# Optimization experiments

Hardware: AMD Instinct MI355X
Metric: run time of the kernel (lower is better)

## Reference

```python
import jax, jax.numpy as jnp
import numpy as np
from jax import lax

E, H = 512, 1024
V_SRC, V_DST = 32000, 32000
T_SRC, T_TGT, B = 64, 64, 64
PAD = 0


def setup_inputs() -> dict:
    key = jax.random.key(0)
    ks = jax.random.split(key, 32)
    def p(i, shape, s=0.02):
        return (jax.random.normal(ks[i], shape) * s).astype(jnp.float32)
    lens = jnp.sort(jax.random.randint(ks[0], (B,), T_SRC // 2, T_SRC + 1))[::-1]
    return {
        "source_padded": jax.random.randint(ks[1], (T_SRC, B), 0, V_SRC).astype(jnp.int32),
        "target_padded": jax.random.randint(ks[2], (T_TGT, B), 0, V_DST).astype(jnp.int32),
        "source_lengths": lens.at[0].set(T_SRC).astype(jnp.int32),
        "src_embed": p(3, (V_SRC, E)),
        "dst_embed": p(4, (V_DST, E)),
        "W_ih_f": p(5, (4 * H, E)), "W_hh_f": p(6, (4 * H, H)),
        "b_ih_f": p(7, (4 * H,)), "b_hh_f": p(8, (4 * H,)),
        "W_ih_b": p(9, (4 * H, E)), "W_hh_b": p(10, (4 * H, H)),
        "b_ih_b": p(11, (4 * H,)), "b_hh_b": p(12, (4 * H,)),
        "W_ih_d": p(13, (4 * H, E + H)), "W_hh_d": p(14, (4 * H, H)),
        "b_ih_d": p(15, (4 * H,)), "b_hh_d": p(16, (4 * H,)),
        "W_hproj": p(17, (H, 2 * H)), "W_cproj": p(18, (H, 2 * H)),
        "W_att": p(19, (H, 2 * H)), "W_comb": p(20, (H, 3 * H)),
        "W_vocab": p(21, (V_DST, H)),
    }


def _lstm_cell(x, h, c, Wih, Whh, bih, bhh):
    # PyTorch gate order: i, f, g, o
    g = x @ Wih.T + bih + h @ Whh.T + bhh
    i, f, gg, o = jnp.split(g, 4, axis=-1)
    c2 = jax.nn.sigmoid(f) * c + jax.nn.sigmoid(i) * jnp.tanh(gg)
    h2 = jax.nn.sigmoid(o) * jnp.tanh(c2)
    return h2, c2


def _nmt_forward(source_padded, target_padded, source_lengths,
                 src_embed, dst_embed,
                 W_ih_f, W_hh_f, b_ih_f, b_hh_f,
                 W_ih_b, W_hh_b, b_ih_b, b_hh_b,
                 W_ih_d, W_hh_d, b_ih_d, b_hh_d,
                 W_hproj, W_cproj, W_att, W_comb, W_vocab):
    T, Bsz = source_padded.shape
    dt = src_embed.dtype
    x = src_embed[source_padded]                      # [T, B, E]
    mask = jnp.arange(T)[:, None] < source_lengths[None, :]  # [T, B] valid

    def make_step(Wih, Whh, bih, bhh):
        def step(carry, inp):
            h, c = carry
            xt, mt = inp
            h2, c2 = _lstm_cell(xt, h, c, Wih, Whh, bih, bhh)
            m = mt[:, None]
            hn = jnp.where(m, h2, h)   # hold state past sequence end (packed semantics)
            cn = jnp.where(m, c2, c)
            return (hn, cn), jnp.where(m, h2, jnp.zeros_like(h2))  # pad outputs are zero
        return step

    z = jnp.zeros((Bsz, H), dt)
    (hf, cf), out_f = lax.scan(make_step(W_ih_f, W_hh_f, b_ih_f, b_hh_f), (z, z), (x, mask))
    (hb, cb), out_b_rev = lax.scan(make_step(W_ih_b, W_hh_b, b_ih_b, b_hh_b), (z, z), (x[::-1], mask[::-1]))
    out_b = out_b_rev[::-1]

    enc_hiddens = jnp.concatenate([out_f, out_b], axis=-1).transpose(1, 0, 2)  # [B, T, 2H]
    h0 = jnp.concatenate([hf, hb], axis=-1) @ W_hproj.T  # [B, H]
    c0 = jnp.concatenate([cf, cb], axis=-1) @ W_cproj.T
    enc_proj = enc_hiddens @ W_att.T                     # [B, T, H]
    pad_mask = ~mask.T                                   # [B, T] True at <pad>

    y = dst_embed[target_padded[:-1]]                    # [Tt-1, B, E]

    def dec_step(carry, yt):
        h, c, o_prev = carry
        ybar = jnp.concatenate([yt, o_prev], axis=-1)    # [B, E+H]
        h2, c2 = _lstm_cell(ybar, h, c, W_ih_d, W_hh_d, b_ih_d, b_hh_d)
        e = jnp.einsum('bth,bh->bt', enc_proj, h2)       # attention scores
        e = jnp.where(pad_mask, -jnp.inf, e)
        alpha = jax.nn.softmax(e, axis=1)
        a = jnp.einsum('bt,btd->bd', alpha, enc_hiddens)  # context [B, 2H]
        O = jnp.tanh(jnp.concatenate([a, h2], axis=-1) @ W_comb.T)  # dropout = identity (eval)
        return (h2, c2, O), O

    _, outs = lax.scan(dec_step, (h0, c0, z), y)         # [Tt-1, B, H]

    P = jax.nn.log_softmax(outs @ W_vocab.T, axis=-1)    # [Tt-1, B, V]
    gold = jnp.take_along_axis(P, target_padded[1:][..., None], axis=-1)[..., 0]
    tmask = (target_padded[1:] != PAD).astype(P.dtype)
    return (gold * tmask).sum(axis=0)                    # [B]


def reference(source_padded, target_padded, source_lengths,
              src_embed, dst_embed,
              W_ih_f, W_hh_f, b_ih_f, b_hh_f,
              W_ih_b, W_hh_b, b_ih_b, b_hh_b,
              W_ih_d, W_hh_d, b_ih_d, b_hh_d,
              W_hproj, W_cproj, W_att, W_comb, W_vocab):
    return _nmt_forward(source_padded, target_padded, source_lengths,
                        src_embed, dst_embed,
                        W_ih_f, W_hh_f, b_ih_f, b_hh_f,
                        W_ih_b, W_hh_b, b_ih_b, b_hh_b,
                        W_ih_d, W_hh_d, b_ih_d, b_hh_d,
                        W_hproj, W_cproj, W_att, W_comb, W_vocab)
```

## Files before the change

### kernel.cpp

```cpp
#include <hip/hip_runtime.h>

typedef __attribute__((ext_vector_type(8))) short short8;
typedef __attribute__((ext_vector_type(4))) float f32x4;
typedef __attribute__((ext_vector_type(4))) unsigned int uint4v;
typedef unsigned short u16;

#define DEVI static __device__ __forceinline__

constexpr int TTm = 64;
constexpr int BBm = 64;
constexpr int EEm = 512;
constexpr int HHm = 1024;
constexpr int GGm = 4096;
constexpr int TDm = 63;

DEVI u16 f2b(float f) {
  unsigned u = __builtin_bit_cast(unsigned, f);
  return (u16)((u + 0x7fffu + ((u >> 16) & 1u)) >> 16);
}
DEVI float b2f(u16 h) { return __builtin_bit_cast(float, (unsigned)h << 16); }
DEVI float sigm(float x) { return 1.0f / (1.0f + __expf(-x)); }
DEVI float tanh_(float x) { return 1.0f - 2.0f / (1.0f + __expf(2.0f * x)); }

DEVI short8 cvt8(const float* p) {
  f32x4 x0 = *(const f32x4*)p;
  f32x4 x1 = *(const f32x4*)(p + 4);
  short8 r;
#pragma unroll
  for (int i = 0; i < 4; ++i) { r[i] = (short)f2b(x0[i]); r[i + 4] = (short)f2b(x1[i]); }
  return r;
}
DEVI void stage32_f32(short* dst, const float* src) {
#pragma unroll
  for (int i = 0; i < 4; ++i) *(short8*)&dst[i * 8] = cvt8(src + i * 8);
}
DEVI void stage32_b16(short* dst, const u16* src) {
#pragma unroll
  for (int i = 0; i < 4; ++i) *(uint4v*)&dst[i * 8] = *(const uint4v*)(src + i * 8);
}

DEVI void gbar(unsigned* flags, unsigned phase) {
  __syncthreads();
  if (threadIdx.x == 0) {
    __builtin_amdgcn_fence(__ATOMIC_RELEASE, "agent");
    __hip_atomic_store(&flags[blockIdx.x * 16], phase, __ATOMIC_RELAXED,
                       __HIP_MEMORY_SCOPE_AGENT);
  }
  if (threadIdx.x < 64) {
    const int i0 = threadIdx.x * 4;
    for (;;) {
      int ok = 1;
#pragma unroll
      for (int i = 0; i < 4; ++i) {
        unsigned v = __hip_atomic_load(&flags[(i0 + i) * 16], __ATOMIC_RELAXED,
                                       __HIP_MEMORY_SCOPE_AGENT);
        ok &= (v >= phase);
      }
      if (__all(ok)) break;
      __builtin_amdgcn_s_sleep(1);
    }
    __builtin_amdgcn_fence(__ATOMIC_ACQUIRE, "agent");
  }
  __syncthreads();
}

DEVI void mfma_bk64(const short* As, const short* Bs, f32x4 acc[4][2], int wv, int ln) {
  const int l15 = ln & 15;
#pragma unroll
  for (int ks = 0; ks < 64; ks += 32) {
    const int kq = ks + ((ln >> 4) << 3);
    short8 b0 = *(const short8*)&Bs[(wv * 32 + l15) * 72 + kq];
    short8 b1 = *(const short8*)&Bs[(wv * 32 + 16 + l15) * 72 + kq];
#pragma unroll
    for (int mt = 0; mt < 4; ++mt) {
      short8 a = *(const short8*)&As[(mt * 16 + l15) * 72 + kq];
      acc[mt][0] = __builtin_amdgcn_mfma_f32_16x16x32_bf16(a, b0, acc[mt][0], 0, 0, 0);
      acc[mt][1] = __builtin_amdgcn_mfma_f32_16x16x32_bf16(a, b1, acc[mt][1], 0, 0, 0);
    }
  }
}

__global__ void k_zero(uint4v* p, int n16) {
  int i = blockIdx.x * blockDim.x + threadIdx.x;
  uint4v z = {0u, 0u, 0u, 0u};
  for (; i < n16; i += gridDim.x * blockDim.x) p[i] = z;
}

__global__ void k_cvt_all(const float* Wihf, const float* Wihb, const float* Whhf,
                          const float* Whhb, const float* Wihd, const float* Whhd,
                          const float* Watt, const float* Whp, const float* Wcp,
                          const float* Wcomb, const float* Wvoc,
                          u16* o_ihf, u16* o_ihb, u16* o_hhf, u16* o_hhb,
                          u16* o_cat1, u16* o_cat2,
                          u16* o_att, u16* o_hp, u16* o_cp, u16* o_comb, u16* o_voc) {
  long i = (long)blockIdx.x * blockDim.x + threadIdx.x;
  const long stride = (long)gridDim.x * blockDim.x;
  for (; i < 65273856L; i += stride) {
    long r = i;
    if (r < 2097152) { o_ihf[r] = f2b(Wihf[r]); continue; } r -= 2097152;
    if (r < 2097152) { o_ihb[r] = f2b(Wihb[r]); continue; } r -= 2097152;
    if (r < 4194304) { o_hhf[r] = f2b(Whhf[r]); continue; } r -= 4194304;
    if (r < 4194304) { o_hhb[r] = f2b(Whhb[r]); continue; } r -= 4194304;
    if (r < 2097152) {
      long g = r >> 9, c = r & 511;
      o_cat1[r] = f2b(Wihd[g * 1536 + c]); continue;
    } r -= 2097152;
    if (r < 8388608) {
      long g = r >> 11, c = r & 2047;
      o_cat2[r] = f2b(c < 1024 ? Wihd[g * 1536 + 512 + c] : Whhd[g * 1024 + (c - 1024)]);
      continue;
    } r -= 8388608;
    if (r < 2097152) { o_att[r] = f2b(Watt[r]); continue; } r -= 2097152;
    if (r < 2097152) { o_hp[r] = f2b(Whp[r]); continue; } r -= 2097152;
    if (r < 2097152) { o_cp[r] = f2b(Wcp[r]); continue; } r -= 2097152;
    if (r < 3145728) { o_comb[r] = f2b(Wcomb[r]); continue; } r -= 3145728;
    o_voc[r] = f2b(Wvoc[r]);
  }
}

__global__ __launch_bounds__(128) void k_pre(
    const int* tok, const float* emb, const u16* W,
    const float* bi, const float* bh, u16* pre) {
  __shared__ short As[64 * 72], Bs[64 * 72];
  const int rt = blockIdx.x, ct = blockIdx.y;
  const int tid = threadIdx.x, wv = tid >> 6, sr = tid & 63, seg = tid >> 6;
  const int token = tok[rt * 64 + sr];
  const float* arow = emb + (long)token * EEm;
  const u16* brow = W + (long)(ct * 64 + sr) * EEm;
  f32x4 acc[4][2] = {};
  for (int k0 = 0; k0 < EEm; k0 += 64) {
    __syncthreads();
    stage32_f32(&As[sr * 72 + seg * 32], arow + k0 + seg * 32);
    stage32_b16(&Bs[sr * 72 + seg * 32], brow + k0 + seg * 32);
    __syncthreads();
    mfma_bk64(As, Bs, acc, wv, sr);
  }
  const int l15 = sr & 15, q = sr >> 4;
#pragma unroll
  for (int nt = 0; nt < 2; ++nt) {
    const int col = ct * 64 + wv * 32 + nt * 16 + l15;
    const float bias = bi[col] + bh[col];
#pragma unroll
    for (int mt = 0; mt < 4; ++mt)
#pragma unroll
      for (int r = 0; r < 4; ++r)
        pre[(long)(rt * 64 + mt * 16 + q * 4 + r) * GGm + col] = f2b(acc[mt][nt][r] + bias);
  }
}

template <bool OUTB16>
__global__ __launch_bounds__(128) void k_gemm_plain(const u16* A, const u16* Bm,
                                                    void* C, int K, int ldb) {
  __shared__ short As[64 * 72], Bs[64 * 72];
  const int rt = blockIdx.x, ct = blockIdx.y;
  const int tid = threadIdx.x, wv = tid >> 6, sr = tid & 63, seg = tid >> 6;
  const u16* arow = A + (long)(rt * 64 + sr) * K;
  const u16* brow = Bm + (long)(ct * 64 + sr) * ldb;
  f32x4 acc[4][2] = {};
  for (int k0 = 0; k0 < K; k0 += 64) {
    __syncthreads();
    stage32_b16(&As[sr * 72 + seg * 32], arow + k0 + seg * 32);
    stage32_b16(&Bs[sr * 72 + seg * 32], brow + k0 + seg * 32);
    __syncthreads();
    mfma_bk64(As, Bs, acc, wv, sr);
  }
  const int l15 = sr & 15, q = sr >> 4, ldc = gridDim.y * 64;
#pragma unroll
  for (int nt = 0; nt < 2; ++nt) {
    const int col = ct * 64 + wv * 32 + nt * 16 + l15;
#pragma unroll
    for (int mt = 0; mt < 4; ++mt)
#pragma unroll
      for (int r = 0; r < 4; ++r) {
        const long idx = (long)(rt * 64 + mt * 16 + q * 4 + r) * ldc + col;
        if (OUTB16) ((u16*)C)[idx] = f2b(acc[mt][nt][r]);
        else        ((float*)C)[idx] = acc[mt][nt][r];
      }
  }
}

__global__ __launch_bounds__(256) void k_enc_all(
    const u16* __restrict__ Whhf, const u16* __restrict__ Whhb,
    const u16* __restrict__ pre_f, const u16* __restrict__ pre_b,
    const int* __restrict__ lens,
    u16* h_f, u16* h_b, u16* ench, u16* hcat, u16* ccat, unsigned* bar) {
  __shared__ float gshE[4 * 64 * 33];
  const int blk = blockIdx.x;
  const int dir = blk >> 7, jt = blk & 127, j0 = jt * 8;
  const u16* Whh = dir ? Whhb : Whhf;
  const u16* pre = dir ? pre_b : pre_f;
  u16* hbase = dir ? h_b : h_f;
  const int tid = threadIdx.x, wv = tid >> 6, ln = tid & 63;
  const int l15 = ln & 15, half = ln >> 4;
  short8 bf[8][2];
#pragma unroll
  for (int i = 0; i < 8; ++i) {
    const int k = (i * 4 + wv) * 32 + half * 8;
#pragma unroll
    for (int nt = 0; nt < 2; ++nt) {
      const int n = nt * 16 + l15, g = n >> 3, jj = n & 7;
      bf[i][nt] = *(const short8*)(Whh + (long)(g * 1024 + j0 + jj) * 1024 + k);
    }
  }
  const int cb = tid & 63, cj = tid >> 6;
  const int len_b = lens[cb];
  float creg[2] = {0.f, 0.f};
  for (int s = 0; s < 64; ++s) {
    const int t = dir ? (63 - s) : s;
    const u16* hcur = hbase + (s & 1) * 65536;
    u16* hnxt = hbase + ((s & 1) ^ 1) * 65536;
    f32x4 acc[4][2] = {};
#pragma unroll
    for (int i = 0; i < 8; ++i) {
      const int k = (i * 4 + wv) * 32 + half * 8;
#pragma unroll
      for (int mt = 0; mt < 4; ++mt) {
        short8 a = *(const short8*)(hcur + (mt * 16 + l15) * 1024 + k);
        acc[mt][0] = __builtin_amdgcn_mfma_f32_16x16x32_bf16(a, bf[i][0], acc[mt][0], 0, 0, 0);
        acc[mt][1] = __builtin_amdgcn_mfma_f32_16x16x32_bf16(a, bf[i][1], acc[mt][1], 0, 0, 0);
      }
    }
    __syncthreads();
#pragma unroll
    for (int mt = 0; mt < 4; ++mt)
#pragma unroll
      for (int nt = 0; nt < 2; ++nt)
#pragma unroll
        for (int r = 0; r < 4; ++r)
          gshE[wv * 2112 + (mt * 16 + half * 4 + r) * 33 + nt * 16 + l15] = acc[mt][nt][r];
    __syncthreads();
#pragma unroll
    for (int u = 0; u < 2; ++u) {
      const int jj = cj + u * 4, j = j0 + jj;
      float g4[4];
#pragma unroll
      for (int g = 0; g < 4; ++g) {
        const int n = g * 8 + jj;
        float v = gshE[cb * 33 + n] + gshE[2112 + cb * 33 + n] +
                  gshE[2 * 2112 + cb * 33 + n] + gshE[3 * 2112 + cb * 33 + n];
        v += b2f(pre[((long)t * 64 + cb) * GGm + g * 1024 + j]);
        g4[g] = v;
      }
      const float cold = creg[u];
      const float c2 = sigm(g4[1]) * cold + sigm(g4[0]) * tanh_(g4[2]);
      const float h2 = sigm(g4[3]) * tanh_(c2);
      const bool m = t < len_b;
      creg[u] = m ? c2 : cold;
      hnxt[cb * 1024 + j] = m ? f2b(h2) : hcur[cb * 1024 + j];
      ench[((long)cb * 64 + t) * 2048 + dir * 1024 + j] = f2b(m ? h2 : 0.f);
    }
    if (s < 63) gbar(bar, s + 1);
  }
#pragma unroll
  for (int u = 0; u < 2; ++u) {
    const int j = j0 + cj + u * 4;
    hcat[cb * 2048 + dir * 1024 + j] = hbase[cb * 1024 + j];
    ccat[cb * 2048 + dir * 1024 + j] = f2b(creg[u]);
  }
}

__global__ __launch_bounds__(256) void k_dec_all(
    const u16* __restrict__ Wcat2, const u16* __restrict__ Wcomb,
    const u16* __restrict__ y_pre, const u16* __restrict__ eproj,
    const u16* __restrict__ encW, const int* __restrict__ lens,
    u16* h_d, float* c_d, u16* o_b, u16* outs, unsigned* bar) {
  __shared__ float gsh[4 * 64 * 17];
  __shared__ float h2s[1024];
  __shared__ float part[256];
  __shared__ float alph[64];
  const int blk = blockIdx.x, tid = threadIdx.x, wv = tid >> 6, ln = tid & 63;
  const int l15 = ln & 15, half = ln >> 4;
  const int j0 = blk * 4;
  short8 bg[16];
#pragma unroll
  for (int i = 0; i < 16; ++i) {
    const int k = (i * 4 + wv) * 32 + half * 8;
    const int g = l15 >> 2, jj = l15 & 3;
    bg[i] = *(const short8*)(Wcat2 + (long)(g * 1024 + j0 + jj) * 2048 + k);
  }
  const int cb = tid & 63, cj = tid >> 6;
  const int ab = blk & 63, aq = blk >> 6;
  const int len_ab = lens[ab];
  float creg = c_d[cb * 1024 + j0 + cj];
  unsigned phase = 0;
  for (int t = 0; t < TDm; ++t) {
    const u16* hprev = h_d + (t & 1) * 65536;
    u16* hnew = h_d + ((t & 1) ^ 1) * 65536;
    f32x4 acc[4] = {};
#pragma unroll
    for (int i = 0; i < 16; ++i) {
      const int k = (i * 4 + wv) * 32 + half * 8;
      const u16* asrc = (k < 1024) ? (o_b + k) : (hprev + (k - 1024));
#pragma unroll
      for (int mt = 0; mt < 4; ++mt) {
        short8 a = *(const short8*)(asrc + (mt * 16 + l15) * 1024);
        acc[mt] = __builtin_amdgcn_mfma_f32_16x16x32_bf16(a, bg[i], acc[mt], 0, 0, 0);
      }
    }
    __syncthreads();
#pragma unroll
    for (int mt = 0; mt < 4; ++mt)
#pragma unroll
      for (int r = 0; r < 4; ++r)
        gsh[wv * 1088 + (mt * 16 + half * 4 + r) * 17 + l15] = acc[mt][r];
    __syncthreads();
    {
      float g4[4];
#pragma unroll
      for (int g = 0; g < 4; ++g) {
        const int n = g * 4 + cj;
        float v = gsh[cb * 17 + n] + gsh[1088 + cb * 17 + n] +
                  gsh[2 * 1088 + cb * 17 + n] + gsh[3 * 1088 + cb * 17 + n];
        v += b2f(y_pre[((long)t * 64 + cb) * GGm + g * 1024 + j0 + cj]);
        g4[g] = v;
      }
      const float c2 = sigm(g4[1]) * creg + sigm(g4[0]) * tanh_(g4[2]);
      const float h2 = sigm(g4[3]) * tanh_(c2);
      creg = c2;
      hnew[cb * 1024 + j0 + cj] = f2b(h2);
    }
    gbar(bar, ++phase);
    for (int i = tid; i < 1024; i += 256) h2s[i] = b2f(hnew[ab * 1024 + i]);
    __syncthreads();
    {
      const int tt = tid >> 2, qq = tid & 3;
      const u16* row = eproj + ((long)ab * 64 + tt) * 1024 + qq * 256;
      float a0 = 0.f;
      for (int i = 0; i < 256; i += 8) {
        uint4v v = *(const uint4v*)(row + i);
        const u16* pv = (const u16*)&v;
#pragma unroll
        for (int j = 0; j < 8; ++j) a0 += b2f(pv[j]) * h2s[qq * 256 + i + j];
      }
      part[tid] = a0;
    }
    __syncthreads();
    if (tid < 64) {
      float e = part[tid * 4] + part[tid * 4 + 1] + part[tid * 4 + 2] + part[tid * 4 + 3];
      e = (tid < len_ab) ? e : -INFINITY;
      float mx = e;
#pragma unroll
      for (int m = 1; m < 64; m <<= 1) mx = fmaxf(mx, __shfl_xor(mx, m));
      float p = __expf(e - mx);
      float s = p;
#pragma unroll
      for (int m = 1; m < 64; m <<= 1) s += __shfl_xor(s, m);
      alph[tid] = p / s;
    }
    __syncthreads();
    {
      const int j = aq * 256 + tid;
      float oa = 0.f;
      for (int tt = 0; tt < 64; ++tt) {
        const float al = alph[tt];
        if (al != 0.f) oa += al * b2f(encW[((long)ab * 64 + tt) * 1024 + j]);
      }
      float oh = 0.f;
      const u16* wrow = Wcomb + (long)j * 3072 + 2048;
      for (int k = 0; k < 1024; k += 8) {
        uint4v v = *(const uint4v*)(wrow + k);
        const u16* pv = (const u16*)&v;
#pragma unroll
        for (int jj = 0; jj < 8; ++jj) oh += b2f(pv[jj]) * h2s[k + jj];
      }
      const u16 ob = f2b(tanh_(oa + oh));
      o_b[ab * 1024 + j] = ob;
      outs[((long)t * 64 + ab) * 1024 + j] = ob;
    }
    if (t < TDm - 1) gbar(bar, ++phase);
  }
}

__global__ __launch_bounds__(128) void k_vocab(const u16* outs, const u16* Wvoc,
                                               float* sumexp) {
  __shared__ short As[64 * 72], Bs[64 * 72];
  const int vt = blockIdx.x, t = blockIdx.y;
  const int tid = threadIdx.x, wv = tid >> 6, sr = tid & 63, seg = tid >> 6;
  const u16* arow = outs + ((long)t * 64 + sr) * 1024;
  const u16* brow = Wvoc + (long)(vt * 64 + sr) * 1024;
  f32x4 acc[4][2] = {};
  for (int k0 = 0; k0 < 1024; k0 += 64) {
    __syncthreads();
    stage32_b16(&As[sr * 72 + seg * 32], arow + k0 + seg * 32);
    stage32_b16(&Bs[sr * 72 + seg * 32], brow + k0 + seg * 32);
    __syncthreads();
    mfma_bk64(As, Bs, acc, wv, sr);
  }
  const int l15 = sr & 15, q = sr >> 4;
#pragma unroll
  for (int mt = 0; mt < 4; ++mt)
#pragma unroll
    for (int r = 0; r < 4; ++r) {
      float e = __expf(acc[mt][0][r]) + __expf(acc[mt][1][r]);
      e += __shfl_xor(e, 1); e += __shfl_xor(e, 2);
      e += __shfl_xor(e, 4); e += __shfl_xor(e, 8);
      if (l15 == 0) atomicAdd(&sumexp[t * 64 + mt * 16 + q * 4 + r], e);
    }
}

__global__ __launch_bounds__(256) void k_gold(const u16* outs, const u16* Wvoc,
                                              const int* tgt, float* gold) {
  const int t = blockIdx.x;
  const int wv = threadIdx.x >> 6, ln = threadIdx.x & 63;
  for (int b = wv; b < 64; b += 4) {
    const int g = tgt[(t + 1) * 64 + b];
    const u16* o = outs + ((long)t * 64 + b) * 1024 + ln * 16;
    const u16* w = Wvoc + (long)g * 1024 + ln * 16;
    uint4v v0 = *(const uint4v*)o, v1 = *(const uint4v*)(o + 8);
    uint4v w0 = *(const uint4v*)w, w1 = *(const uint4v*)(w + 8);
    const u16 *pv0 = (const u16*)&v0, *pv1 = (const u16*)&v1;
    const u16 *pw0 = (const u16*)&w0, *pw1 = (const u16*)&w1;
    float acc = 0.f;
#pragma unroll
    for (int j = 0; j < 8; ++j)
      acc += b2f(pv0[j]) * b2f(pw0[j]) + b2f(pv1[j]) * b2f(pw1[j]);
#pragma unroll
    for (int m = 1; m < 64; m <<= 1) acc += __shfl_xor(acc, m);
    if (ln == 0) gold[t * 64 + b] = acc;
  }
}

__global__ void k_final(const float* gold, const float* sumexp, const int* tgt,
                        float* out) {
  const int b = threadIdx.x;
  float s = 0.f;
  for (int t = 0; t < TDm; ++t)
    if (tgt[(t + 1) * 64 + b] != 0)
      s += gold[t * 64 + b] - logf(sumexp[t * 64 + b]);
  out[b] = s;
}

extern "C" void kernel_launch(void* const* d_in, const int* in_sizes, int n_in,
                              void* d_out, int out_size, void* d_ws, size_t ws_size,
                              hipStream_t stream) {
  const int* src_tok = (const int*)d_in[0];
  const int* tgt_tok = (const int*)d_in[1];
  const int* lens    = (const int*)d_in[2];
  const float* semb  = (const float*)d_in[3];
  const float* demb  = (const float*)d_in[4];
  const float* Wihf  = (const float*)d_in[5];
  const float* Whhf  = (const float*)d_in[6];
  const float* bihf  = (const float*)d_in[7];
  const float* bhhf  = (const float*)d_in[8];
  const float* Wihb  = (const float*)d_in[9];
  const float* Whhb  = (const float*)d_in[10];
  const float* bihb  = (const float*)d_in[11];
  const float* bhhb  = (const float*)d_in[12];
  const float* Wihd  = (const float*)d_in[13];
  const float* Whhd  = (const float*)d_in[14];
  const float* bihd  = (const float*)d_in[15];
  const float* bhhd  = (const float*)d_in[16];
  const float* Whp   = (const float*)d_in[17];
  const float* Wcp   = (const float*)d_in[18];
  const float* Watt  = (const float*)d_in[19];
  const float* Wcomb = (const float*)d_in[20];
  const float* Wvoc  = (const float*)d_in[21];

  char* w = (char*)d_ws;
  auto alloc = [&](size_t bytes) { char* p = w; w += (bytes + 255) & ~(size_t)255; return p; };
  u16* h_f    = (u16*)alloc(262144);
  u16* h_b    = (u16*)alloc(262144);
  u16* o_b    = (u16*)alloc(131072);
  float* sume = (float*)alloc(16384);
  unsigned* barE = (unsigned*)alloc(16384);
  unsigned* barD = (unsigned*)alloc(16384);
  const int zero16 = (int)((w - (char*)h_f) / 16);
  float* gold   = (float*)alloc(16384);
  float* c_d    = (float*)alloc(262144);
  u16* h_d      = (u16*)alloc(262144);
  u16* hcat     = (u16*)alloc(262144);
  u16* ccat     = (u16*)alloc(262144);
  u16* Wb_ihf   = (u16*)alloc(4194304);
  u16* Wb_ihb   = (u16*)alloc(4194304);
  u16* Wb_hhf   = (u16*)alloc(8388608);
  u16* Wb_hhb   = (u16*)alloc(8388608);
  u16* Wb_cat1  = (u16*)alloc(4194304);
  u16* Wb_cat2  = (u16*)alloc(16777216);
  u16* Wb_att   = (u16*)alloc(4194304);
  u16* Wb_hp    = (u16*)alloc(4194304);
  u16* Wb_cp    = (u16*)alloc(4194304);
  u16* Wb_comb  = (u16*)alloc(6291456);
  u16* Wb_voc   = (u16*)alloc(65536000);
  u16* pre_f    = (u16*)alloc(33554432);
  u16* pre_b    = (u16*)alloc(33554432);
  u16* y_pre    = (u16*)alloc(33030144);
  u16* ench     = (u16*)alloc(16777216);
  u16* eproj    = (u16*)alloc(8388608);
  u16* encW     = (u16*)alloc(8388608);
  u16* outs     = (u16*)alloc(8257536);

  k_zero<<<dim3(128), dim3(256), 0, stream>>>((uint4v*)h_f, zero16);
  k_cvt_all<<<dim3(2048), dim3(256), 0, stream>>>(
      Wihf, Wihb, Whhf, Whhb, Wihd, Whhd, Watt, Whp, Wcp, Wcomb, Wvoc,
      Wb_ihf, Wb_ihb, Wb_hhf, Wb_hhb, Wb_cat1, Wb_cat2,
      Wb_att, Wb_hp, Wb_cp, Wb_comb, Wb_voc);
  k_pre<<<dim3(64, 64), dim3(128), 0, stream>>>(src_tok, semb, Wb_ihf, bihf, bhhf, pre_f);
  k_pre<<<dim3(64, 64), dim3(128), 0, stream>>>(src_tok, semb, Wb_ihb, bihb, bhhb, pre_b);
  k_pre<<<dim3(63, 64), dim3(128), 0, stream>>>(tgt_tok, demb, Wb_cat1, bihd, bhhd, y_pre);
  {
    void* args[] = {(void*)&Wb_hhf, (void*)&Wb_hhb, (void*)&pre_f, (void*)&pre_b,
                    (void*)&lens, (void*)&h_f, (void*)&h_b, (void*)&ench,
                    (void*)&hcat, (void*)&ccat, (void*)&barE};
    hipLaunchCooperativeKernel((void*)k_enc_all, dim3(256), dim3(256), args, 0, stream);
  }
  k_gemm_plain<true><<<dim3(1, 16), dim3(128), 0, stream>>>(hcat, Wb_hp, (void*)h_d, 2048, 2048);
  k_gemm_plain<false><<<dim3(1, 16), dim3(128), 0, stream>>>(ccat, Wb_cp, (void*)c_d, 2048, 2048);
  k_gemm_plain<true><<<dim3(64, 16), dim3(128), 0, stream>>>(ench, Wb_att, (void*)eproj, 2048, 2048);
  k_gemm_plain<true><<<dim3(64, 16), dim3(128), 0, stream>>>(ench, Wb_comb, (void*)encW, 2048, 3072);
  {
    void* args[] = {(void*)&Wb_cat2, (void*)&Wb_comb, (void*)&y_pre, (void*)&eproj,
                    (void*)&encW, (void*)&lens, (void*)&h_d, (void*)&c_d,
                    (void*)&o_b, (void*)&outs, (void*)&barD};
    hipLaunchCooperativeKernel((void*)k_dec_all, dim3(256), dim3(256), args, 0, stream);
  }
  k_vocab<<<dim3(500, 63), dim3(128), 0, stream>>>(outs, Wb_voc, sume);
  k_gold<<<dim3(63), dim3(256), 0, stream>>>(outs, Wb_voc, tgt_tok, gold);
  k_final<<<dim3(1), dim3(64), 0, stream>>>(gold, sume, tgt_tok, (float*)d_out);
}
```

Before: 9.233 ms.

## Replace fence-based grid barrier with write-through stores and per-step history buffers

Recurrent state buffers (encoder h, decoder h and o) change from ping-pong double buffers to full per-timestep history arrays, so each step writes to fresh addresses that no other block has cached. Cross-block stores go out as write-through system-scope global_store_short (sc0 sc1), which lets the grid barrier drop its agent-scope release and acquire fences in favour of a vmcnt wait. The intent is to cut the cache writeback and invalidate cost of the 64+126 grid barriers in the recurrent loops. In exchange it uses more workspace and relies on the fresh-address argument for correctness, since readers no longer do an acquire invalidate. The outs buffer now aliases the decoder o-history.

```diff
diff --git a/kernel.cpp b/kernel.cpp
--- a/kernel.cpp
+++ b/kernel.cpp
@@ -39,10 +39,15 @@
   for (int i = 0; i < 4; ++i) *(uint4v*)&dst[i * 8] = *(const uint4v*)(src + i * 8);
 }
 
+DEVI void st_sys_b16(u16* p, u16 v) {
+  unsigned d = v;
+  asm volatile("global_store_short %0, %1, off sc0 sc1" :: "v"(p), "v"(d) : "memory");
+}
+
 DEVI void gbar(unsigned* flags, unsigned phase) {
+  asm volatile("s_waitcnt vmcnt(0)" ::: "memory");
   __syncthreads();
   if (threadIdx.x == 0) {
-    __builtin_amdgcn_fence(__ATOMIC_RELEASE, "agent");
     __hip_atomic_store(&flags[blockIdx.x * 16], phase, __ATOMIC_RELAXED,
                        __HIP_MEMORY_SCOPE_AGENT);
   }
@@ -59,8 +64,8 @@
       if (__all(ok)) break;
       __builtin_amdgcn_s_sleep(1);
     }
-    __builtin_amdgcn_fence(__ATOMIC_ACQUIRE, "agent");
-  }
+  }
+  asm volatile("" ::: "memory");
   __syncthreads();
 }
 
@@ -183,13 +188,13 @@
     const u16* __restrict__ Whhf, const u16* __restrict__ Whhb,
     const u16* __restrict__ pre_f, const u16* __restrict__ pre_b,
     const int* __restrict__ lens,
-    u16* h_f, u16* h_b, u16* ench, u16* hcat, u16* ccat, unsigned* bar) {
+    u16* hist_f, u16* hist_b, u16* ench, u16* hcat, u16* ccat, unsigned* bar) {
   __shared__ float gshE[4 * 64 * 33];
   const int blk = blockIdx.x;
   const int dir = blk >> 7, jt = blk & 127, j0 = jt * 8;
   const u16* Whh = dir ? Whhb : Whhf;
   const u16* pre = dir ? pre_b : pre_f;
-  u16* hbase = dir ? h_b : h_f;
+  u16* hist = dir ? hist_b : hist_f;
   const int tid = threadIdx.x, wv = tid >> 6, ln = tid & 63;
   const int l15 = ln & 15, half = ln >> 4;
   short8 bf[8][2];
@@ -205,10 +210,11 @@
   const int cb = tid & 63, cj = tid >> 6;
   const int len_b = lens[cb];
   float creg[2] = {0.f, 0.f};
+  u16 hlast[2] = {0, 0};
   for (int s = 0; s < 64; ++s) {
     const int t = dir ? (63 - s) : s;
-    const u16* hcur = hbase + (s & 1) * 65536;
-    u16* hnxt = hbase + ((s & 1) ^ 1) * 65536;
+    const u16* hcur = hist + s * 65536;
+    u16* hnxt = hist + (s + 1) * 65536;
     f32x4 acc[4][2] = {};
 #pragma unroll
     for (int i = 0; i < 8; ++i) {
@@ -246,7 +252,9 @@
       const float h2 = sigm(g4[3]) * tanh_(c2);
       const bool m = t < len_b;
       creg[u] = m ? c2 : cold;
-      hnxt[cb * 1024 + j] = m ? f2b(h2) : hcur[cb * 1024 + j];
+      const u16 hv = m ? f2b(h2) : hcur[cb * 1024 + j];
+      if (s < 63) st_sys_b16(&hnxt[cb * 1024 + j], hv);
+      else        hlast[u] = hv;
       ench[((long)cb * 64 + t) * 2048 + dir * 1024 + j] = f2b(m ? h2 : 0.f);
     }
     if (s < 63) gbar(bar, s + 1);
@@ -254,7 +262,7 @@
 #pragma unroll
   for (int u = 0; u < 2; ++u) {
     const int j = j0 + cj + u * 4;
-    hcat[cb * 2048 + dir * 1024 + j] = hbase[cb * 1024 + j];
+    hcat[cb * 2048 + dir * 1024 + j] = hlast[u];
     ccat[cb * 2048 + dir * 1024 + j] = f2b(creg[u]);
   }
 }
@@ -263,7 +271,7 @@
     const u16* __restrict__ Wcat2, const u16* __restrict__ Wcomb,
     const u16* __restrict__ y_pre, const u16* __restrict__ eproj,
     const u16* __restrict__ encW, const int* __restrict__ lens,
-    u16* h_d, float* c_d, u16* o_b, u16* outs, unsigned* bar) {
+    u16* h_hist, const float* c_d, u16* o_hist, unsigned* bar) {
   __shared__ float gsh[4 * 64 * 17];
   __shared__ float h2s[1024];
   __shared__ float part[256];
@@ -284,13 +292,15 @@
   float creg = c_d[cb * 1024 + j0 + cj];
   unsigned phase = 0;
   for (int t = 0; t < TDm; ++t) {
-    const u16* hprev = h_d + (t & 1) * 65536;
-    u16* hnew = h_d + ((t & 1) ^ 1) * 65536;
+    const u16* hprev = h_hist + t * 65536;
+    u16* hnew = h_hist + (t + 1) * 65536;
+    const u16* o_prev = o_hist + t * 65536;
+    u16* o_out = o_hist + (t + 1) * 65536;
     f32x4 acc[4] = {};
 #pragma unroll
     for (int i = 0; i < 16; ++i) {
       const int k = (i * 4 + wv) * 32 + half * 8;
-      const u16* asrc = (k < 1024) ? (o_b + k) : (hprev + (k - 1024));
+      const u16* asrc = (k < 1024) ? (o_prev + k) : (hprev + (k - 1024));
 #pragma unroll
       for (int mt = 0; mt < 4; ++mt) {
         short8 a = *(const short8*)(asrc + (mt * 16 + l15) * 1024);
@@ -317,7 +327,7 @@
       const float c2 = sigm(g4[1]) * creg + sigm(g4[0]) * tanh_(g4[2]);
       const float h2 = sigm(g4[3]) * tanh_(c2);
       creg = c2;
-      hnew[cb * 1024 + j0 + cj] = f2b(h2);
+      st_sys_b16(&hnew[cb * 1024 + j0 + cj], f2b(h2));
     }
     gbar(bar, ++phase);
     for (int i = tid; i < 1024; i += 256) h2s[i] = b2f(hnew[ab * 1024 + i]);
@@ -364,8 +374,7 @@
         for (int jj = 0; jj < 8; ++jj) oh += b2f(pv[jj]) * h2s[k + jj];
       }
       const u16 ob = f2b(tanh_(oa + oh));
-      o_b[ab * 1024 + j] = ob;
-      outs[((long)t * 64 + ab) * 1024 + j] = ob;
+      st_sys_b16(&o_out[ab * 1024 + j], ob);
     }
     if (t < TDm - 1) gbar(bar, ++phase);
   }
@@ -458,16 +467,16 @@
 
   char* w = (char*)d_ws;
   auto alloc = [&](size_t bytes) { char* p = w; w += (bytes + 255) & ~(size_t)255; return p; };
-  u16* h_f    = (u16*)alloc(262144);
-  u16* h_b    = (u16*)alloc(262144);
-  u16* o_b    = (u16*)alloc(131072);
+  u16* histF  = (u16*)alloc(8388608);
+  u16* histB  = (u16*)alloc(8388608);
+  u16* o_hist = (u16*)alloc(8388608);
   float* sume = (float*)alloc(16384);
   unsigned* barE = (unsigned*)alloc(16384);
   unsigned* barD = (unsigned*)alloc(16384);
-  const int zero16 = (int)((w - (char*)h_f) / 16);
+  const int zero16 = (int)((w - (char*)histF) / 16);
   float* gold   = (float*)alloc(16384);
   float* c_d    = (float*)alloc(262144);
-  u16* h_d      = (u16*)alloc(262144);
+  u16* h_hist   = (u16*)alloc(8388608);
   u16* hcat     = (u16*)alloc(262144);
   u16* ccat     = (u16*)alloc(262144);
   u16* Wb_ihf   = (u16*)alloc(4194304);
@@ -487,9 +496,9 @@
   u16* ench     = (u16*)alloc(16777216);
   u16* eproj    = (u16*)alloc(8388608);
   u16* encW     = (u16*)alloc(8388608);
-  u16* outs     = (u16*)alloc(8257536);
-
-  k_zero<<<dim3(128), dim3(256), 0, stream>>>((uint4v*)h_f, zero16);
+  u16* outs     = o_hist + 65536;
+
+  k_zero<<<dim3(256), dim3(256), 0, stream>>>((uint4v*)histF, zero16);
   k_cvt_all<<<dim3(2048), dim3(256), 0, stream>>>(
       Wihf, Wihb, Whhf, Whhb, Wihd, Whhd, Watt, Whp, Wcp, Wcomb, Wvoc,
       Wb_ihf, Wb_ihb, Wb_hhf, Wb_hhb, Wb_cat1, Wb_cat2,
@@ -499,18 +508,18 @@
   k_pre<<<dim3(63, 64), dim3(128), 0, stream>>>(tgt_tok, demb, Wb_cat1, bihd, bhhd, y_pre);
   {
     void* args[] = {(void*)&Wb_hhf, (void*)&Wb_hhb, (void*)&pre_f, (void*)&pre_b,
-                    (void*)&lens, (void*)&h_f, (void*)&h_b, (void*)&ench,
+                    (void*)&lens, (void*)&histF, (void*)&histB, (void*)&ench,
                     (void*)&hcat, (void*)&ccat, (void*)&barE};
     hipLaunchCooperativeKernel((void*)k_enc_all, dim3(256), dim3(256), args, 0, stream);
   }
-  k_gemm_plain<true><<<dim3(1, 16), dim3(128), 0, stream>>>(hcat, Wb_hp, (void*)h_d, 2048, 2048);
+  k_gemm_plain<true><<<dim3(1, 16), dim3(128), 0, stream>>>(hcat, Wb_hp, (void*)h_hist, 2048, 2048);
   k_gemm_plain<false><<<dim3(1, 16), dim3(128), 0, stream>>>(ccat, Wb_cp, (void*)c_d, 2048, 2048);
   k_gemm_plain<true><<<dim3(64, 16), dim3(128), 0, stream>>>(ench, Wb_att, (void*)eproj, 2048, 2048);
   k_gemm_plain<true><<<dim3(64, 16), dim3(128), 0, stream>>>(ench, Wb_comb, (void*)encW, 2048, 3072);
   {
     void* args[] = {(void*)&Wb_cat2, (void*)&Wb_comb, (void*)&y_pre, (void*)&eproj,
-                    (void*)&encW, (void*)&lens, (void*)&h_d, (void*)&c_d,
-                    (void*)&o_b, (void*)&outs, (void*)&barD};
+                    (void*)&encW, (void*)&lens, (void*)&h_hist, (void*)&c_d,
+                    (void*)&o_hist, (void*)&barD};
     hipLaunchCooperativeKernel((void*)k_dec_all, dim3(256), dim3(256), args, 0, stream);
   }
   k_vocab<<<dim3(500, 63), dim3(128), 0, stream>>>(outs, Wb_voc, sume);
```

Result: faster. 7.883 ms (-14.6%).
